# Kernel optimization log

Measured on AMD Instinct MI355X. Metric: run time of the kernel, lower is better.

The kernel has to match this reference:

```python
import jax, jax.numpy as jnp
import numpy as np

B, Q = 4, 65536
LATENT = 256
FEAT = 32
RES = 64
HID = [256, 256, 256]
TRIDIM = 3 * FEAT * RES * RES  # 393216


def _bilinear_sample(plane, xy):
    """F.grid_sample equivalent: bilinear, padding_mode='border', align_corners=True.
    plane: [C, H, W]; xy: [Q, 2] with xy[:,0]=x (width), xy[:,1]=y (height), in [-1,1].
    Returns [Q, C]."""
    C, H, W = plane.shape
    x = (xy[:, 0] + 1.0) * 0.5 * (W - 1)  # align_corners=True mapping
    y = (xy[:, 1] + 1.0) * 0.5 * (H - 1)
    x0 = jnp.floor(x)
    y0 = jnp.floor(y)
    wx = x - x0
    wy = y - y0
    x0i = jnp.clip(x0.astype(jnp.int32), 0, W - 1)
    x1i = jnp.clip(x0i + 1, 0, W - 1)  # border padding via clamp
    y0i = jnp.clip(y0.astype(jnp.int32), 0, H - 1)
    y1i = jnp.clip(y0i + 1, 0, H - 1)
    v00 = plane[:, y0i, x0i]  # [C, Q]
    v01 = plane[:, y0i, x1i]
    v10 = plane[:, y1i, x0i]
    v11 = plane[:, y1i, x1i]
    top = v00 * (1.0 - wx) + v01 * wx
    bot = v10 * (1.0 - wx) + v11 * wx
    return (top * (1.0 - wy) + bot * wy).T  # [Q, C]


def _sample_triplanes(triplanes, pts):
    """triplanes: [3, C, R, R]; pts: [Q, 3] clamped to [-1,1]. Returns [Q, 3C]."""
    xy = _bilinear_sample(triplanes[0], pts[:, jnp.array([0, 1])])
    xz = _bilinear_sample(triplanes[1], pts[:, jnp.array([0, 2])])
    yz = _bilinear_sample(triplanes[2], pts[:, jnp.array([1, 2])])
    return jnp.concatenate([xy, xz, yz], axis=-1)


def setup_inputs() -> dict:
    key = jax.random.key(0)
    ks = jax.random.split(key, 20)
    d_in_mlp = 3 * FEAT + 3  # 99

    def lin(k, i, o):
        k1, k2 = jax.random.split(k)
        s = 1.0 / np.sqrt(i)
        return (jax.random.uniform(k1, (i, o), jnp.float32, -s, s),
                jax.random.uniform(k2, (o,), jnp.float32, -s, s))

    w1, b1 = lin(ks[0], LATENT, 2 * LATENT)
    w2, b2 = lin(ks[1], 2 * LATENT, TRIDIM)
    mw0, mb0 = lin(ks[2], d_in_mlp, HID[0])
    mw1, mb1 = lin(ks[3], HID[0], HID[1])
    mw2, mb2 = lin(ks[4], HID[1], HID[2])
    sdf_w, sdf_b = lin(ks[5], HID[2], 1)
    occ_w, occ_b = lin(ks[6], HID[2], 1)

    z_sample = jax.random.normal(ks[7], (B, LATENT), jnp.float32)
    query_points = jax.random.uniform(ks[8], (B, Q, 3), jnp.float32) * 2.0 - 1.0

    return {"z_sample": z_sample, "query_points": query_points,
            "w1": w1, "b1": b1, "w2": w2, "b2": b2,
            "mw0": mw0, "mb0": mb0, "mw1": mw1, "mb1": mb1,
            "mw2": mw2, "mb2": mb2,
            "sdf_w": sdf_w, "sdf_b": sdf_b, "occ_w": occ_w, "occ_b": occ_b}


def reference(z_sample, query_points, w1, b1, w2, b2, mw0, mb0, mw1, mb1,
              mw2, mb2, sdf_w, sdf_b, occ_w, occ_b):
    # triplane head: Linear -> SiLU -> Linear, reshaped to [B, 3, C, R, R]
    h = jax.nn.silu(z_sample @ w1 + b1)
    triplanes = (h @ w2 + b2).reshape(B, 3, FEAT, RES, RES)

    pts = jnp.clip(query_points, -1.0, 1.0)  # clamp only for sampling
    query_feats = jax.vmap(_sample_triplanes)(triplanes, pts)  # [B, Q, 3C]

    x = jnp.concatenate([query_feats, query_points], axis=-1)  # [B, Q, 3C+3]
    x = jax.nn.silu(x @ mw0 + mb0)
    x = jax.nn.silu(x @ mw1 + mb1)
    x = jax.nn.silu(x @ mw2 + mb2)
    sdf_pred = x @ sdf_w + sdf_b
    occ_logits = x @ occ_w + occ_b
    return triplanes, sdf_pred, occ_logits
```

## Files before the change

kernel.cpp:

```cpp
#include <hip/hip_runtime.h>
#include <cstdint>

#define BQ 4
#define QPB 65536
#define QTOT (BQ*QPB)
#define TRIN 393216
#define TRI_OUT (BQ*TRIN)

#define X0LD 272
#define ACTLD 528

typedef __attribute__((ext_vector_type(8))) __bf16 bf16x8;
typedef __attribute__((ext_vector_type(4))) float f32x4;

__device__ __forceinline__ unsigned short f2bf(float f) {
    unsigned u = __float_as_uint(f);
    u += 0x7fffu + ((u >> 16) & 1u);
    return (unsigned short)(u >> 16);
}
__device__ __forceinline__ float bflo(unsigned u) {
    return __uint_as_float(u << 16);
}
__device__ __forceinline__ float bfhi(unsigned u) {
    return __uint_as_float(u & 0xffff0000u);
}
__device__ __forceinline__ unsigned cvt_pk_bf16(float lo, float hi) {
    unsigned r;
    asm("v_cvt_pk_bf16_f32 %0, %1, %2" : "=v"(r) : "v"(lo), "v"(hi));
    return r;
}
__device__ __forceinline__ float fast_rcp(float d) {
    float r;
    asm("v_rcp_f32 %0, %1" : "=v"(r) : "v"(d));
    return r;
}
__device__ __forceinline__ float silu_f(float x) {
    return x * fast_rcp(1.0f + __expf(-x));
}
__device__ __forceinline__ int c_true(int p) {
    return (p & ~63) + ((p & 3) * 16 + ((p & 63) >> 2));
}

__global__ __launch_bounds__(256) void k_prep_w(
    const float* __restrict__ mw0, const float* __restrict__ mw1, const float* __restrict__ mw2,
    const float* __restrict__ sdf_w, const float* __restrict__ occ_w,
    unsigned short* __restrict__ wt0, unsigned short* __restrict__ wt1,
    unsigned short* __restrict__ wt2, float* __restrict__ sdfp, float* __restrict__ occp)
{
    int idx = blockIdx.x * 256 + threadIdx.x;
    if (idx < 163840) {
        const float* src;
        unsigned short* dst;
        int rel;
        bool perm;
        int kmax;
        if (idx < 32768)       { rel = idx;         src = mw0; dst = wt0; perm = false; kmax = 99;  }
        else if (idx < 98304)  { rel = idx - 32768; src = mw1; dst = wt1; perm = true;  kmax = 256; }
        else                   { rel = idx - 98304; src = mw2; dst = wt2; perm = true;  kmax = 256; }
        int e  = rel & 7;
        int kg = (rel >> 3) & 3;
        int n  = (rel >> 5) & 255;
        int t  = rel >> 13;
        int ks = t * 32 + kg * 8 + e;
        int k  = perm ? c_true(ks) : ks;
        float v = (ks < kmax) ? src[k * 256 + n] : 0.0f;
        dst[rel] = f2bf(v);
    } else if (idx < 164352) {
        int r = idx - 163840;
        int p = r & 255, which = r >> 8;
        float v = (which ? occ_w : sdf_w)[c_true(p)];
        (which ? occp : sdfp)[p] = v;
    }
}

__global__ __launch_bounds__(256) void k_h(
    const float* __restrict__ z, const float* __restrict__ w1,
    const float* __restrict__ b1, float* __restrict__ hout)
{
    int gid = blockIdx.x * 256 + threadIdx.x;
    int b = gid >> 9, n = gid & 511;
    float acc = b1[n];
    #pragma unroll 8
    for (int k = 0; k < 256; ++k)
        acc += z[b * 256 + k] * w1[k * 512 + n];
    hout[gid] = silu_f(acc);
}

__global__ __launch_bounds__(256) void k_triplane(
    const float* __restrict__ w2, const float* __restrict__ b2,
    const float* __restrict__ h, float* __restrict__ outTri,
    unsigned short* __restrict__ triT)
{
    __shared__ float hs[2048];
    int t = threadIdx.x;
    ((float4*)hs)[t]       = ((const float4*)h)[t];
    ((float4*)hs)[t + 256] = ((const float4*)h)[t + 256];
    __syncthreads();
    int g = blockIdx.x * 256 + t;
    int j = g * 2;
    const float* wj = w2 + j;
    float ax[4] = {0.f, 0.f, 0.f, 0.f}, ay[4] = {0.f, 0.f, 0.f, 0.f};

    for (int k0 = 0; k0 < 512; k0 += 8) {
        float2 wv[8];
        #pragma unroll
        for (int u = 0; u < 8; ++u)
            wv[u] = *(const float2*)(wj + (size_t)(k0 + u) * TRIN);
        float4 hv[4][2];
        #pragma unroll
        for (int b = 0; b < 4; ++b) {
            hv[b][0] = *(const float4*)&hs[b * 512 + k0];
            hv[b][1] = *(const float4*)&hs[b * 512 + k0 + 4];
        }
        #pragma unroll
        for (int b = 0; b < 4; ++b) {
            ax[b] += hv[b][0].x * wv[0].x + hv[b][0].y * wv[1].x
                   + hv[b][0].z * wv[2].x + hv[b][0].w * wv[3].x
                   + hv[b][1].x * wv[4].x + hv[b][1].y * wv[5].x
                   + hv[b][1].z * wv[6].x + hv[b][1].w * wv[7].x;
            ay[b] += hv[b][0].x * wv[0].y + hv[b][0].y * wv[1].y
                   + hv[b][0].z * wv[2].y + hv[b][0].w * wv[3].y
                   + hv[b][1].x * wv[4].y + hv[b][1].y * wv[5].y
                   + hv[b][1].z * wv[6].y + hv[b][1].w * wv[7].y;
        }
    }

    float2 bj = *(const float2*)(b2 + j);
    int x = j & 63, y = (j >> 6) & 63, c = (j >> 12) & 31, p = j >> 17;
    int ttb = ((p * 64 + y) * 64 + x) * 32 + c;
    #pragma unroll
    for (int b = 0; b < 4; ++b) {
        float vX = ax[b] + bj.x, vY = ay[b] + bj.y;
        float2 o; o.x = vX; o.y = vY;
        *(float2*)(outTri + (size_t)b * TRIN + j) = o;
        unsigned short* tb = triT + b * TRIN + ttb;
        tb[0]  = f2bf(vX);
        tb[32] = f2bf(vY);
    }
}

template<int K, bool INPLACE, int LDIN>
__device__ __forceinline__ void mlp_layer(
    const unsigned char* bin, unsigned char* bout,
    const unsigned short* __restrict__ wtp, const float* __restrict__ mb,
    int lane, int c4)
{
    const int l15 = lane & 15;
    const int kg = lane >> 4;
    const int n0 = c4 * 64;
    const unsigned char* abase = bin + l15 * LDIN + kg * 16;
    f32x4 acc[4][4];
    #pragma unroll
    for (int rf = 0; rf < 4; ++rf)
        #pragma unroll
        for (int cf = 0; cf < 4; ++cf) {
            f32x4 zv = {0.f, 0.f, 0.f, 0.f};
            acc[rf][cf] = zv;
        }
    #pragma unroll
    for (int t = 0; t < K / 32; ++t) {
        uint4 av[4], bv[4];
        #pragma unroll
        for (int rf = 0; rf < 4; ++rf)
            av[rf] = *(const uint4*)(abase + rf * 16 * LDIN + t * 64);
        #pragma unroll
        for (int cf = 0; cf < 4; ++cf) {
            int n = n0 + 16 * cf + l15;
            bv[cf] = *(const uint4*)(wtp + (((t * 256 + n) * 4 + kg) << 3));
        }
        __builtin_amdgcn_s_setprio(1);
        #pragma unroll
        for (int rf = 0; rf < 4; ++rf)
            #pragma unroll
            for (int cf = 0; cf < 4; ++cf)
                acc[rf][cf] = __builtin_amdgcn_mfma_f32_16x16x32_bf16(
                    __builtin_bit_cast(bf16x8, av[rf]),
                    __builtin_bit_cast(bf16x8, bv[cf]),
                    acc[rf][cf], 0, 0, 0);
        __builtin_amdgcn_s_setprio(0);
    }
    if (INPLACE) __syncthreads();
    float bias[4];
    #pragma unroll
    for (int cf = 0; cf < 4; ++cf) bias[cf] = mb[n0 + 16 * cf + l15];
    unsigned char* sbase = bout + kg * 4 * ACTLD + (n0 + l15 * 4) * 2;
    #pragma unroll
    for (int rf = 0; rf < 4; ++rf) {
        #pragma unroll
        for (int jj = 0; jj < 4; ++jj) {
            float v0 = silu_f(acc[rf][0][jj] + bias[0]);
            float v1 = silu_f(acc[rf][1][jj] + bias[1]);
            float v2 = silu_f(acc[rf][2][jj] + bias[2]);
            float v3 = silu_f(acc[rf][3][jj] + bias[3]);
            uint2 pk;
            pk.x = cvt_pk_bf16(v0, v1);
            pk.y = cvt_pk_bf16(v2, v3);
            *(uint2*)(sbase + (rf * 16 + jj) * ACTLD) = pk;
        }
    }
    __syncthreads();
}

__global__ __launch_bounds__(256) void k_mlp(
    const float* __restrict__ qp, const unsigned short* __restrict__ triT,
    const unsigned short* __restrict__ wt0, const unsigned short* __restrict__ wt1,
    const unsigned short* __restrict__ wt2,
    const float* __restrict__ mb0, const float* __restrict__ mb1, const float* __restrict__ mb2,
    const float* __restrict__ sdfp, const float* __restrict__ sdf_b,
    const float* __restrict__ occp, const float* __restrict__ occ_b,
    float* __restrict__ out)
{
    __shared__ __align__(16) unsigned char lds[64 * X0LD + 64 * ACTLD];
    unsigned char* x0  = lds;
    unsigned char* act = lds + 64 * X0LD;
    unsigned char* scr = act;
    const int t = threadIdx.x;

    const int bid = blockIdx.x;
    const int xcd = bid & 7;
    const int batch = xcd >> 1;
    const int brow = (bid >> 3) + ((xcd & 1) << 9);
    const int row0 = batch * QPB + brow * 64;

    if (t < 192) {
        int plane = t >> 6, q = t & 63;
        int gr = row0 + q;
        float px = qp[3 * gr], py = qp[3 * gr + 1], pz = qp[3 * gr + 2];
        float u = (plane == 2) ? py : px;
        float v = (plane == 0) ? py : pz;
        u = fminf(fmaxf(u, -1.f), 1.f);
        v = fminf(fmaxf(v, -1.f), 1.f);
        float xf = (u + 1.f) * 31.5f;
        float yf = (v + 1.f) * 31.5f;
        float x0f = floorf(xf), y0f = floorf(yf);
        float wx = xf - x0f, wy = yf - y0f;
        int xi = min(max((int)x0f, 0), 63);
        int yi = min(max((int)y0f, 0), 63);
        int xi1 = min(xi + 1, 63), yi1 = min(yi + 1, 63);
        int pb = (batch * 3 + plane) * 64;
        int4 offs;
        offs.x = ((pb + yi ) * 64 + xi ) << 6;
        offs.y = ((pb + yi ) * 64 + xi1) << 6;
        offs.z = ((pb + yi1) * 64 + xi ) << 6;
        offs.w = ((pb + yi1) * 64 + xi1) << 6;
        float4 w;
        w.x = (1.f - wx) * (1.f - wy); w.y = wx * (1.f - wy);
        w.z = (1.f - wx) * wy;         w.w = wx * wy;
        *(int4*)(scr + t * 32) = offs;
        *(float4*)(scr + t * 32 + 16) = w;
        if (plane == 0) {
            uint4 c0;
            c0.x = (unsigned)f2bf(px) | ((unsigned)f2bf(py) << 16);
            c0.y = (unsigned)f2bf(pz);
            c0.z = 0u; c0.w = 0u;
            uint4 z4; z4.x = z4.y = z4.z = z4.w = 0u;
            *(uint4*)(x0 + q * X0LD + 192) = c0;
            *(uint4*)(x0 + q * X0LD + 208) = z4;
            *(uint4*)(x0 + q * X0LD + 224) = z4;
            *(uint4*)(x0 + q * X0LD + 240) = z4;
        }
    }
    __syncthreads();

    const char* tb8 = (const char*)triT;
    #pragma unroll
    for (int i = 0; i < 3; ++i) {
        int unit = i * 256 + t;
        int chunk = unit & 3;
        int uc = unit >> 2;
        const unsigned char* ce = scr + uc * 32;
        int4 offs = *(const int4*)ce;
        float4 w = *(const float4*)(ce + 16);
        int cb = chunk * 16;
        uint4 c0 = *(const uint4*)(tb8 + offs.x + cb);
        uint4 c1 = *(const uint4*)(tb8 + offs.y + cb);
        uint4 c2 = *(const uint4*)(tb8 + offs.z + cb);
        uint4 c3 = *(const uint4*)(tb8 + offs.w + cb);
        const unsigned* u0 = (const unsigned*)&c0;
        const unsigned* u1 = (const unsigned*)&c1;
        const unsigned* u2 = (const unsigned*)&c2;
        const unsigned* u3 = (const unsigned*)&c3;
        unsigned r[4];
        #pragma unroll
        for (int q2 = 0; q2 < 4; ++q2) {
            float lo = w.x * bflo(u0[q2]) + w.y * bflo(u1[q2])
                     + w.z * bflo(u2[q2]) + w.w * bflo(u3[q2]);
            float hi = w.x * bfhi(u0[q2]) + w.y * bfhi(u1[q2])
                     + w.z * bfhi(u2[q2]) + w.w * bfhi(u3[q2]);
            r[q2] = cvt_pk_bf16(lo, hi);
        }
        int q = uc & 63, plane = uc >> 6;
        uint4 pk; pk.x = r[0]; pk.y = r[1]; pk.z = r[2]; pk.w = r[3];
        *(uint4*)(x0 + q * X0LD + plane * 64 + chunk * 16) = pk;
    }
    __syncthreads();

    const int lane = t & 63;
    const int c4 = t >> 6;

    mlp_layer<128, false, X0LD >(x0,  act, wt0, mb0, lane, c4);
    mlp_layer<256, true,  ACTLD>(act, act, wt1, mb1, lane, c4);
    mlp_layer<256, true,  ACTLD>(act, act, wt2, mb2, lane, c4);

    {
        const int l15 = lane & 15;
        const int kg = lane >> 4;
        int row = c4 * 16 + l15;
        int gr = row0 + row;
        const unsigned char* hbase = act + row * ACTLD + kg * 128;
        float aS = 0.f, aO = 0.f;
        int kb = kg * 64;
        #pragma unroll
        for (int i = 0; i < 8; ++i) {
            int k = kb + i * 8;
            uint4 xv = *(const uint4*)(hbase + i * 16);
            const unsigned* xu = (const unsigned*)&xv;
            float4 s0 = *(const float4*)(sdfp + k);
            float4 s1 = *(const float4*)(sdfp + k + 4);
            float4 o0 = *(const float4*)(occp + k);
            float4 o1 = *(const float4*)(occp + k + 4);
            float xr[8];
            #pragma unroll
            for (int q = 0; q < 4; ++q) {
                xr[2 * q]     = bflo(xu[q]);
                xr[2 * q + 1] = bfhi(xu[q]);
            }
            aS += xr[0] * s0.x + xr[1] * s0.y + xr[2] * s0.z + xr[3] * s0.w
                + xr[4] * s1.x + xr[5] * s1.y + xr[6] * s1.z + xr[7] * s1.w;
            aO += xr[0] * o0.x + xr[1] * o0.y + xr[2] * o0.z + xr[3] * o0.w
                + xr[4] * o1.x + xr[5] * o1.y + xr[6] * o1.z + xr[7] * o1.w;
        }
        aS += __shfl_xor(aS, 16);
        aS += __shfl_xor(aS, 32);
        aO += __shfl_xor(aO, 16);
        aO += __shfl_xor(aO, 32);
        if (kg == 0) {
            out[TRI_OUT + gr] = aS + sdf_b[0];
            out[TRI_OUT + QTOT + gr] = aO + occ_b[0];
        }
    }
}

extern "C" void kernel_launch(void* const* d_in, const int* in_sizes, int n_in,
                              void* d_out, int out_size, void* d_ws, size_t ws_size,
                              hipStream_t stream)
{
    const float* z     = (const float*)d_in[0];
    const float* qp    = (const float*)d_in[1];
    const float* w1    = (const float*)d_in[2];
    const float* b1    = (const float*)d_in[3];
    const float* w2    = (const float*)d_in[4];
    const float* b2    = (const float*)d_in[5];
    const float* mw0   = (const float*)d_in[6];
    const float* mb0   = (const float*)d_in[7];
    const float* mw1   = (const float*)d_in[8];
    const float* mb1   = (const float*)d_in[9];
    const float* mw2   = (const float*)d_in[10];
    const float* mb2   = (const float*)d_in[11];
    const float* sdf_w = (const float*)d_in[12];
    const float* sdf_b = (const float*)d_in[13];
    const float* occ_w = (const float*)d_in[14];
    const float* occ_b = (const float*)d_in[15];
    float* out = (float*)d_out;
    char* ws = (char*)d_ws;

    float* h_ws          = (float*)(ws);
    unsigned short* wt0  = (unsigned short*)(ws + 8192);
    unsigned short* wt1  = (unsigned short*)(ws + 73728);
    unsigned short* wt2  = (unsigned short*)(ws + 204800);
    float* sdfp          = (float*)(ws + 335872);
    float* occp          = (float*)(ws + 336896);
    unsigned short* triT = (unsigned short*)(ws + 337920);

    k_prep_w<<<643, 256, 0, stream>>>(mw0, mw1, mw2, sdf_w, occ_w,
                                      wt0, wt1, wt2, sdfp, occp);
    k_h<<<8, 256, 0, stream>>>(z, w1, b1, h_ws);
    k_triplane<<<768, 256, 0, stream>>>(w2, b2, h_ws, out, triT);
    k_mlp<<<4096, 256, 0, stream>>>(qp, triT, wt0, wt1, wt2,
                                    mb0, mb1, mb2, sdfp, sdf_b, occp, occ_b, out);
}
```

Measured before the change: 304.8 us.

## Split MLP rows per wave to drop inter-layer barriers and shrink LDS

The MLP layers are repartitioned so each wave owns 16 full rows across all 256 output columns, instead of all 64 rows for a 64-column slice. Because each wave only ever reads and writes its own rows, the layers run in place with no __syncthreads between them. The separate input buffer and scratch area are folded into the single activation buffer, which cuts LDS use per block and may allow more blocks per CU. In exchange, every wave now loads the full weight tile from global memory per k-step, roughly four times more weight traffic through the caches, and there is less A-operand reuse.

```diff
diff --git a/kernel.cpp b/kernel.cpp
--- a/kernel.cpp
+++ b/kernel.cpp
@@ -7,7 +7,6 @@
 #define TRIN 393216
 #define TRI_OUT (BQ*TRIN)
 
-#define X0LD 272
 #define ACTLD 528
 
 typedef __attribute__((ext_vector_type(8))) __bf16 bf16x8;
@@ -139,66 +138,57 @@
     }
 }
 
-template<int K, bool INPLACE, int LDIN>
-__device__ __forceinline__ void mlp_layer(
-    const unsigned char* bin, unsigned char* bout,
+template<int K>
+__device__ __forceinline__ void mlp_layer_w(
+    unsigned char* act,
     const unsigned short* __restrict__ wtp, const float* __restrict__ mb,
-    int lane, int c4)
+    int wid, int lane)
 {
     const int l15 = lane & 15;
     const int kg = lane >> 4;
-    const int n0 = c4 * 64;
-    const unsigned char* abase = bin + l15 * LDIN + kg * 16;
-    f32x4 acc[4][4];
-    #pragma unroll
-    for (int rf = 0; rf < 4; ++rf)
-        #pragma unroll
-        for (int cf = 0; cf < 4; ++cf) {
-            f32x4 zv = {0.f, 0.f, 0.f, 0.f};
-            acc[rf][cf] = zv;
-        }
+    const unsigned char* abase = act + (wid * 16 + l15) * ACTLD + kg * 16;
+    f32x4 acc[16];
+    #pragma unroll
+    for (int cf = 0; cf < 16; ++cf) {
+        f32x4 zv = {0.f, 0.f, 0.f, 0.f};
+        acc[cf] = zv;
+    }
     #pragma unroll
     for (int t = 0; t < K / 32; ++t) {
-        uint4 av[4], bv[4];
-        #pragma unroll
-        for (int rf = 0; rf < 4; ++rf)
-            av[rf] = *(const uint4*)(abase + rf * 16 * LDIN + t * 64);
-        #pragma unroll
-        for (int cf = 0; cf < 4; ++cf) {
-            int n = n0 + 16 * cf + l15;
-            bv[cf] = *(const uint4*)(wtp + (((t * 256 + n) * 4 + kg) << 3));
-        }
-        __builtin_amdgcn_s_setprio(1);
-        #pragma unroll
-        for (int rf = 0; rf < 4; ++rf)
+        uint4 av = *(const uint4*)(abase + t * 64);
+        #pragma unroll
+        for (int cg = 0; cg < 4; ++cg) {
+            uint4 bv[4];
             #pragma unroll
-            for (int cf = 0; cf < 4; ++cf)
-                acc[rf][cf] = __builtin_amdgcn_mfma_f32_16x16x32_bf16(
-                    __builtin_bit_cast(bf16x8, av[rf]),
-                    __builtin_bit_cast(bf16x8, bv[cf]),
-                    acc[rf][cf], 0, 0, 0);
-        __builtin_amdgcn_s_setprio(0);
-    }
-    if (INPLACE) __syncthreads();
-    float bias[4];
-    #pragma unroll
-    for (int cf = 0; cf < 4; ++cf) bias[cf] = mb[n0 + 16 * cf + l15];
-    unsigned char* sbase = bout + kg * 4 * ACTLD + (n0 + l15 * 4) * 2;
-    #pragma unroll
-    for (int rf = 0; rf < 4; ++rf) {
-        #pragma unroll
-        for (int jj = 0; jj < 4; ++jj) {
-            float v0 = silu_f(acc[rf][0][jj] + bias[0]);
-            float v1 = silu_f(acc[rf][1][jj] + bias[1]);
-            float v2 = silu_f(acc[rf][2][jj] + bias[2]);
-            float v3 = silu_f(acc[rf][3][jj] + bias[3]);
+            for (int c4 = 0; c4 < 4; ++c4) {
+                int n = cg * 64 + c4 * 16 + l15;
+                bv[c4] = *(const uint4*)(wtp + (((t * 256 + n) * 4 + kg) << 3));
+            }
+            __builtin_amdgcn_s_setprio(1);
+            #pragma unroll
+            for (int c4 = 0; c4 < 4; ++c4)
+                acc[cg * 4 + c4] = __builtin_amdgcn_mfma_f32_16x16x32_bf16(
+                    __builtin_bit_cast(bf16x8, av),
+                    __builtin_bit_cast(bf16x8, bv[c4]),
+                    acc[cg * 4 + c4], 0, 0, 0);
+            __builtin_amdgcn_s_setprio(0);
+        }
+    }
+    unsigned char* sbase = act + (wid * 16 + kg * 4) * ACTLD + l15 * 8;
+    #pragma unroll
+    for (int jj = 0; jj < 4; ++jj) {
+        #pragma unroll
+        for (int g = 0; g < 4; ++g) {
+            float v0 = silu_f(acc[g * 4 + 0][jj] + mb[(g * 4 + 0) * 16 + l15]);
+            float v1 = silu_f(acc[g * 4 + 1][jj] + mb[(g * 4 + 1) * 16 + l15]);
+            float v2 = silu_f(acc[g * 4 + 2][jj] + mb[(g * 4 + 2) * 16 + l15]);
+            float v3 = silu_f(acc[g * 4 + 3][jj] + mb[(g * 4 + 3) * 16 + l15]);
             uint2 pk;
             pk.x = cvt_pk_bf16(v0, v1);
             pk.y = cvt_pk_bf16(v2, v3);
-            *(uint2*)(sbase + (rf * 16 + jj) * ACTLD) = pk;
-        }
-    }
-    __syncthreads();
+            *(uint2*)(sbase + jj * ACTLD + g * 128) = pk;
+        }
+    }
 }
 
 __global__ __launch_bounds__(256) void k_mlp(
@@ -210,10 +200,8 @@
     const float* __restrict__ occp, const float* __restrict__ occ_b,
     float* __restrict__ out)
 {
-    __shared__ __align__(16) unsigned char lds[64 * X0LD + 64 * ACTLD];
-    unsigned char* x0  = lds;
-    unsigned char* act = lds + 64 * X0LD;
-    unsigned char* scr = act;
+    __shared__ __align__(16) unsigned char act[64 * ACTLD];
+    #define SCR(u) (act + ((u) >> 3) * ACTLD + 256 + ((u) & 7) * 32)
     const int t = threadIdx.x;
 
     const int bid = blockIdx.x;
@@ -246,18 +234,18 @@
         float4 w;
         w.x = (1.f - wx) * (1.f - wy); w.y = wx * (1.f - wy);
         w.z = (1.f - wx) * wy;         w.w = wx * wy;
-        *(int4*)(scr + t * 32) = offs;
-        *(float4*)(scr + t * 32 + 16) = w;
+        *(int4*)SCR(t) = offs;
+        *(float4*)(SCR(t) + 16) = w;
         if (plane == 0) {
             uint4 c0;
             c0.x = (unsigned)f2bf(px) | ((unsigned)f2bf(py) << 16);
             c0.y = (unsigned)f2bf(pz);
             c0.z = 0u; c0.w = 0u;
             uint4 z4; z4.x = z4.y = z4.z = z4.w = 0u;
-            *(uint4*)(x0 + q * X0LD + 192) = c0;
-            *(uint4*)(x0 + q * X0LD + 208) = z4;
-            *(uint4*)(x0 + q * X0LD + 224) = z4;
-            *(uint4*)(x0 + q * X0LD + 240) = z4;
+            *(uint4*)(act + q * ACTLD + 192) = c0;
+            *(uint4*)(act + q * ACTLD + 208) = z4;
+            *(uint4*)(act + q * ACTLD + 224) = z4;
+            *(uint4*)(act + q * ACTLD + 240) = z4;
         }
     }
     __syncthreads();
@@ -268,7 +256,7 @@
         int unit = i * 256 + t;
         int chunk = unit & 3;
         int uc = unit >> 2;
-        const unsigned char* ce = scr + uc * 32;
+        const unsigned char* ce = SCR(uc);
         int4 offs = *(const int4*)ce;
         float4 w = *(const float4*)(ce + 16);
         int cb = chunk * 16;
@@ -291,21 +279,21 @@
         }
         int q = uc & 63, plane = uc >> 6;
         uint4 pk; pk.x = r[0]; pk.y = r[1]; pk.z = r[2]; pk.w = r[3];
-        *(uint4*)(x0 + q * X0LD + plane * 64 + chunk * 16) = pk;
+        *(uint4*)(act + q * ACTLD + plane * 64 + chunk * 16) = pk;
     }
     __syncthreads();
 
     const int lane = t & 63;
-    const int c4 = t >> 6;
-
-    mlp_layer<128, false, X0LD >(x0,  act, wt0, mb0, lane, c4);
-    mlp_layer<256, true,  ACTLD>(act, act, wt1, mb1, lane, c4);
-    mlp_layer<256, true,  ACTLD>(act, act, wt2, mb2, lane, c4);
+    const int wid = t >> 6;
+
+    mlp_layer_w<128>(act, wt0, mb0, wid, lane);
+    mlp_layer_w<256>(act, wt1, mb1, wid, lane);
+    mlp_layer_w<256>(act, wt2, mb2, wid, lane);
 
     {
         const int l15 = lane & 15;
         const int kg = lane >> 4;
-        int row = c4 * 16 + l15;
+        int row = wid * 16 + l15;
         int gr = row0 + row;
         const unsigned char* hbase = act + row * ACTLD + kg * 128;
         float aS = 0.f, aO = 0.f;
@@ -339,6 +327,7 @@
             out[TRI_OUT + QTOT + gr] = aO + occ_b[0];
         }
     }
+    #undef SCR
 }
 
 extern "C" void kernel_launch(void* const* d_in, const int* in_sizes, int n_in,
```

After: 504.8 us. 1.66x slower.
